# Kernel tuning notes

Measured on AMD Instinct MI355X. Metric: run time of the kernel, lower is better.

Reference implementation:

```python
import jax, jax.numpy as jnp
import numpy as np

H = 50  # hidden size hard-coded in the torch module


def _lstm_layer(x, W_ih, W_hh, b_ih, b_hh):
    """x: [B, T, D_in] -> outputs [B, T, H]. PyTorch gate order: i, f, g, o."""
    B = x.shape[0]
    # precompute input projection for all timesteps: [B, T, 4H]
    x_proj = jnp.einsum('btd,gd->btg', x, W_ih) + b_ih + b_hh
    x_proj = jnp.swapaxes(x_proj, 0, 1)  # time-major [T, B, 4H]

    def step(carry, xt):
        h, c = carry
        gates = xt + h @ W_hh.T  # [B, 4H]
        i, f, g, o = jnp.split(gates, 4, axis=-1)
        c = jax.nn.sigmoid(f) * c + jax.nn.sigmoid(i) * jnp.tanh(g)
        h = jax.nn.sigmoid(o) * jnp.tanh(c)
        return (h, c), h

    h0 = jnp.zeros((B, H), dtype=x.dtype)
    c0 = jnp.zeros((B, H), dtype=x.dtype)
    (_, _), hs = jax.lax.scan(step, (h0, c0), x_proj)
    return jnp.swapaxes(hs, 0, 1)  # [B, T, H]


def setup_inputs() -> dict:
    key = jax.random.key(0)
    ks = jax.random.split(key, 11)
    B, T = 4096, 512
    s = 1.0 / np.sqrt(H)  # torch LSTM init scale
    return {
        'x': jax.random.normal(ks[0], (B, T, 1), dtype=jnp.float32),
        'W_ih0': jax.random.normal(ks[1], (4 * H, 1), dtype=jnp.float32) * s,
        'W_hh0': jax.random.normal(ks[2], (4 * H, H), dtype=jnp.float32) * s,
        'b_ih0': jax.random.normal(ks[3], (4 * H,), dtype=jnp.float32) * s,
        'b_hh0': jax.random.normal(ks[4], (4 * H,), dtype=jnp.float32) * s,
        'W_ih1': jax.random.normal(ks[5], (4 * H, H), dtype=jnp.float32) * s,
        'W_hh1': jax.random.normal(ks[6], (4 * H, H), dtype=jnp.float32) * s,
        'b_ih1': jax.random.normal(ks[7], (4 * H,), dtype=jnp.float32) * s,
        'b_hh1': jax.random.normal(ks[8], (4 * H,), dtype=jnp.float32) * s,
        'W_fc': jax.random.normal(ks[9], (1, H), dtype=jnp.float32) * s,
        'b_fc': jax.random.normal(ks[10], (1,), dtype=jnp.float32) * s,
    }


def reference(x, W_ih0, W_hh0, b_ih0, b_hh0, W_ih1, W_hh1, b_ih1, b_hh1, W_fc, b_fc):
    h1 = _lstm_layer(x, W_ih0, W_hh0, b_ih0, b_hh0)   # [B, T, H]
    h2 = _lstm_layer(h1, W_ih1, W_hh1, b_ih1, b_hh1)  # [B, T, H]
    last = h2[:, -1, :]                                # [B, H]
    return last @ W_fc.T + b_fc                        # [B, 1]
```

## Files before the change

### kernel.cpp

```cpp
#include <hip/hip_runtime.h>


#define TT 512
#define HH 50
#define BT 16
#define NTHR 832
#define L2E 1.44269504f

typedef _Float16 half8 __attribute__((ext_vector_type(8)));
typedef float floatx4 __attribute__((ext_vector_type(4)));

static __device__ __forceinline__ float fexp2(float x) { return __builtin_amdgcn_exp2f(x); }
static __device__ __forceinline__ float frcp(float x)  { return __builtin_amdgcn_rcpf(x); }

static __device__ __forceinline__ float cell_update(float gi, float gf, float gg,
                                                    float go, float& c) {
    float Ei = fexp2(gi);
    float Eg = fexp2(gg);
    float Ef = fexp2(gf);
    float p1 = (1.0f + Ei) * (1.0f + Eg);
    float fe = 1.0f + Ef;
    float R  = frcp(fe * p1);
    c = R * (c * p1 + (1.0f - Eg) * fe);
    float cl = fminf(fmaxf(c, -18.0f), 18.0f);
    float Eo = fexp2(go);
    float Ec = fexp2(cl * (-2.0f * L2E));
    float Ro = frcp((1.0f + Eo) * (1.0f + Ec));
    return (1.0f - Ec) * Ro;
}

#define MFMA(a, b, c) __builtin_amdgcn_mfma_f32_16x16x32_f16((a), (b), (c), 0, 0, 0)

__global__ __launch_bounds__(NTHR, 4) void lstm_mfma(
    const float* __restrict__ x,
    const float* __restrict__ W_ih0, const float* __restrict__ W_hh0,
    const float* __restrict__ b_ih0, const float* __restrict__ b_hh0,
    const float* __restrict__ W_ih1, const float* __restrict__ W_hh1,
    const float* __restrict__ b_ih1, const float* __restrict__ b_hh1,
    const float* __restrict__ W_fc,  const float* __restrict__ b_fc,
    float* __restrict__ out)
{
    __shared__ __align__(16) _Float16 Hf[2][2048];
    __shared__ float xs[TT * BT];

    const int tid = threadIdx.x;
    const int ln  = tid & 63;
    const int wv  = tid >> 6;
    const int m   = ln & 15;
    const int q   = ln >> 4;
    const int b0g = blockIdx.x * BT;

    const float GSC[4] = { -L2E, -L2E, -2.0f * L2E, -L2E };

    for (int i = tid; i < BT * TT; i += NTHR) {
        int b = i & 15, t = i >> 4;
        xs[t * BT + b] = x[(size_t)(b0g + b) * TT + t];
    }
    for (int i = tid; i < 2 * 2048; i += NTHR) ((_Float16*)Hf)[i] = (_Float16)0.f;

    const int  uA   = 4 * wv + (m >> 2);
    const int  gA   = m & 3;
    const bool rokA = (uA < HH);
    const int  wrow = gA * HH + uA;
    const float sA  = GSC[gA];

    half8 a0[2];
    half8 a1[4];
#pragma unroll
    for (int ks = 0; ks < 2; ++ks) {
        half8 h8;
#pragma unroll
        for (int j = 0; j < 8; ++j) {
            int k = ks * 32 + q * 8 + j;
            float w = (rokA && k < HH) ? W_hh0[wrow * HH + k] : 0.f;
            h8[j] = (_Float16)(sA * w);
        }
        a0[ks] = h8;
    }
#pragma unroll
    for (int ks = 0; ks < 4; ++ks) {
        half8 h8;
#pragma unroll
        for (int j = 0; j < 8; ++j) {
            int k = ks * 32 + q * 8 + j;
            float w = 0.f;
            if (rokA) {
                if (k < HH)                      w = W_ih1[wrow * HH + k];
                else if (k >= 64 && k < 64 + HH) w = W_hh1[wrow * HH + (k - 64)];
            }
            h8[j] = (_Float16)(sA * w);
        }
        a1[ks] = h8;
    }

    const int  uC = 4 * wv + q;
    const bool vC = (uC < HH);
    float cc0[4], bw0[4], cc1[4];
#pragma unroll
    for (int g = 0; g < 4; ++g) {
        int rg = g * HH + (vC ? uC : 0);
        cc0[g] = vC ? GSC[g] * (b_ih0[rg] + b_hh0[rg]) : 0.f;
        bw0[g] = vC ? GSC[g] * W_ih0[rg] : 0.f;
        cc1[g] = vC ? GSC[g] * (b_ih1[rg] + b_hh1[rg]) : 0.f;
    }
    const int kh = uC & 63;
    const int widx = ((kh >> 5) * 64 + ((kh >> 3) & 3) * 16 + m) * 8 + (kh & 7);
    float c1 = 0.f, c2 = 0.f;

    __syncthreads();

#define ITER(ttv, P, DO_L0)                                               \
    {                                                                     \
        half8 b0 = *(const half8*)&Hf[(P)][(0 * 64 + ln) * 8];            \
        half8 b1 = *(const half8*)&Hf[(P)][(1 * 64 + ln) * 8];            \
        half8 b2 = *(const half8*)&Hf[(P)][(2 * 64 + ln) * 8];            \
        half8 b3 = *(const half8*)&Hf[(P)][(3 * 64 + ln) * 8];            \
        if (DO_L0) {                                                      \
            const float xv = xs[(ttv) * BT + m];                          \
            floatx4 acc;                                                  \
            _Pragma("unroll")                                             \
            for (int g = 0; g < 4; ++g) acc[g] = cc0[g] + bw0[g] * xv;    \
            acc = MFMA(a0[0], b0, acc);                                   \
            acc = MFMA(a0[1], b1, acc);                                   \
            float h = cell_update(acc[0], acc[1], acc[2], acc[3], c1);    \
            Hf[(P) ^ 1][widx] = (_Float16)h;                              \
        }                                                                 \
        {                                                                 \
            floatx4 acc;                                                  \
            _Pragma("unroll")                                             \
            for (int g = 0; g < 4; ++g) acc[g] = cc1[g];                  \
            acc = MFMA(a1[0], b0, acc);                                   \
            acc = MFMA(a1[1], b1, acc);                                   \
            acc = MFMA(a1[2], b2, acc);                                   \
            acc = MFMA(a1[3], b3, acc);                                   \
            float h = cell_update(acc[0], acc[1], acc[2], acc[3], c2);    \
            Hf[(P) ^ 1][widx + 1024] = (_Float16)h;                       \
        }                                                                 \
        __syncthreads();                                                  \
    }

    {
        const float xv = xs[m];
        float h = cell_update(cc0[0] + bw0[0] * xv, cc0[1] + bw0[1] * xv,
                              cc0[2] + bw0[2] * xv, cc0[3] + bw0[3] * xv, c1);
        Hf[1][widx] = (_Float16)h;
        __syncthreads();
    }

    for (int k = 1; k <= 255; ++k) {
        ITER(2 * k - 1, 1, true);
        ITER(2 * k,     0, true);
    }
    ITER(511, 1, true);
    ITER(512, 0, false);

    if (tid < BT) {
        float a = b_fc[0];
        for (int u = 0; u < HH; ++u) {
            int k = 64 + u;
            int idx = ((k >> 5) * 64 + ((k >> 3) & 3) * 16 + tid) * 8 + (k & 7);
            a = fmaf((float)Hf[1][idx], W_fc[u], a);
        }
        out[b0g + tid] = a;
    }
#undef ITER
}

extern "C" void kernel_launch(void* const* d_in, const int* in_sizes, int n_in,
                              void* d_out, int out_size, void* d_ws, size_t ws_size,
                              hipStream_t stream) {
    const float* x     = (const float*)d_in[0];
    const float* W_ih0 = (const float*)d_in[1];
    const float* W_hh0 = (const float*)d_in[2];
    const float* b_ih0 = (const float*)d_in[3];
    const float* b_hh0 = (const float*)d_in[4];
    const float* W_ih1 = (const float*)d_in[5];
    const float* W_hh1 = (const float*)d_in[6];
    const float* b_ih1 = (const float*)d_in[7];
    const float* b_hh1 = (const float*)d_in[8];
    const float* W_fc  = (const float*)d_in[9];
    const float* b_fc  = (const float*)d_in[10];
    float* out = (float*)d_out;

    dim3 grid(4096 / BT);
    dim3 block(NTHR);
    lstm_mfma<<<grid, block, 0, stream>>>(x, W_ih0, W_hh0, b_ih0, b_hh0,
                                          W_ih1, W_hh1, b_ih1, b_hh1,
                                          W_fc, b_fc, out);
}
```

Measured before the change: 409.0 us.

## Specialize waves per LSTM layer with multiple hidden-unit tiles per wave

```diff
diff --git a/kernel.cpp b/kernel.cpp
--- a/kernel.cpp
+++ b/kernel.cpp
@@ -4,7 +4,7 @@
 #define TT 512
 #define HH 50
 #define BT 16
-#define NTHR 832
+#define NTHR 512
 #define L2E 1.44269504f
 
 typedef _Float16 half8 __attribute__((ext_vector_type(8)));
@@ -31,7 +31,182 @@
 
 #define MFMA(a, b, c) __builtin_amdgcn_mfma_f32_16x16x32_f16((a), (b), (c), 0, 0, 0)
 
-__global__ __launch_bounds__(NTHR, 4) void lstm_mfma(
+template<int NJ>
+static __device__ __forceinline__ void run_l0(
+    int tbase, int ln, _Float16 (*Hf)[2048], const float* xs,
+    const float* __restrict__ W_ih0, const float* __restrict__ W_hh0,
+    const float* __restrict__ b_ih0, const float* __restrict__ b_hh0)
+{
+    const int m = ln & 15, q = ln >> 4;
+    const float GSC[4] = { -L2E, -L2E, -2.0f * L2E, -L2E };
+
+    half8 a0[NJ][2];
+    float cc0[NJ][4], bw0[NJ][4], c[NJ];
+    int   widx[NJ];
+#pragma unroll
+    for (int j = 0; j < NJ; ++j) {
+        const int  tau  = tbase + j;
+        const int  uA   = 4 * tau + (m >> 2);
+        const int  gA   = m & 3;
+        const bool rokA = (uA < HH);
+        const int  wrow = gA * HH + uA;
+        const float sA  = GSC[gA];
+#pragma unroll
+        for (int ks = 0; ks < 2; ++ks) {
+            half8 h8;
+#pragma unroll
+            for (int jj = 0; jj < 8; ++jj) {
+                int k = ks * 32 + q * 8 + jj;
+                float w = (rokA && k < HH) ? W_hh0[wrow * HH + k] : 0.f;
+                h8[jj] = (_Float16)(sA * w);
+            }
+            a0[j][ks] = h8;
+        }
+        const int  uC = 4 * tau + q;
+        const bool vC = (uC < HH);
+#pragma unroll
+        for (int g = 0; g < 4; ++g) {
+            int rg = g * HH + (vC ? uC : 0);
+            cc0[j][g] = vC ? GSC[g] * (b_ih0[rg] + b_hh0[rg]) : 0.f;
+            bw0[j][g] = vC ? GSC[g] * W_ih0[rg] : 0.f;
+        }
+        const int kh = uC & 63;
+        widx[j] = ((kh >> 5) * 64 + ((kh >> 3) & 3) * 16 + m) * 8 + (kh & 7);
+        c[j] = 0.f;
+    }
+
+    __syncthreads();
+
+    {
+        const float xv = xs[m];
+#pragma unroll
+        for (int j = 0; j < NJ; ++j) {
+            float h = cell_update(cc0[j][0] + bw0[j][0] * xv, cc0[j][1] + bw0[j][1] * xv,
+                                  cc0[j][2] + bw0[j][2] * xv, cc0[j][3] + bw0[j][3] * xv,
+                                  c[j]);
+            Hf[1][widx[j]] = (_Float16)h;
+        }
+        __syncthreads();
+    }
+
+#define ITER0(ttv, P)                                                       \
+    {                                                                       \
+        half8 b0 = *(const half8*)&Hf[(P)][(0 * 64 + ln) * 8];              \
+        half8 b1 = *(const half8*)&Hf[(P)][(1 * 64 + ln) * 8];              \
+        const float xv = xs[(ttv) * BT + m];                                \
+        floatx4 acc[NJ];                                                    \
+        _Pragma("unroll")                                                   \
+        for (int j = 0; j < NJ; ++j) {                                      \
+            floatx4 a;                                                      \
+            _Pragma("unroll")                                               \
+            for (int g = 0; g < 4; ++g) a[g] = cc0[j][g] + bw0[j][g] * xv;  \
+            a = MFMA(a0[j][0], b0, a);                                      \
+            a = MFMA(a0[j][1], b1, a);                                      \
+            acc[j] = a;                                                     \
+        }                                                                   \
+        _Pragma("unroll")                                                   \
+        for (int j = 0; j < NJ; ++j) {                                      \
+            float h = cell_update(acc[j][0], acc[j][1], acc[j][2], acc[j][3], c[j]); \
+            Hf[(P) ^ 1][widx[j]] = (_Float16)h;                             \
+        }                                                                   \
+        __syncthreads();                                                    \
+    }
+
+    for (int k = 1; k <= 255; ++k) {
+        ITER0(2 * k - 1, 1);
+        ITER0(2 * k, 0);
+    }
+    ITER0(511, 1);
+    __syncthreads();
+#undef ITER0
+}
+
+template<int NJ>
+static __device__ __forceinline__ void run_l1(
+    int tbase, int ln, _Float16 (*Hf)[2048],
+    const float* __restrict__ W_ih1, const float* __restrict__ W_hh1,
+    const float* __restrict__ b_ih1, const float* __restrict__ b_hh1)
+{
+    const int m = ln & 15, q = ln >> 4;
+    const float GSC[4] = { -L2E, -L2E, -2.0f * L2E, -L2E };
+
+    half8 a1[NJ][4];
+    float cc1[NJ][4], c[NJ];
+    int   widx[NJ];
+#pragma unroll
+    for (int j = 0; j < NJ; ++j) {
+        const int  tau  = tbase + j;
+        const int  uA   = 4 * tau + (m >> 2);
+        const int  gA   = m & 3;
+        const bool rokA = (uA < HH);
+        const int  wrow = gA * HH + uA;
+        const float sA  = GSC[gA];
+#pragma unroll
+        for (int ks = 0; ks < 4; ++ks) {
+            half8 h8;
+#pragma unroll
+            for (int jj = 0; jj < 8; ++jj) {
+                int k = ks * 32 + q * 8 + jj;
+                float w = 0.f;
+                if (rokA) {
+                    if (k < HH)                      w = W_ih1[wrow * HH + k];
+                    else if (k >= 64 && k < 64 + HH) w = W_hh1[wrow * HH + (k - 64)];
+                }
+                h8[jj] = (_Float16)(sA * w);
+            }
+            a1[j][ks] = h8;
+        }
+        const int  uC = 4 * tau + q;
+        const bool vC = (uC < HH);
+#pragma unroll
+        for (int g = 0; g < 4; ++g) {
+            int rg = g * HH + (vC ? uC : 0);
+            cc1[j][g] = vC ? GSC[g] * (b_ih1[rg] + b_hh1[rg]) : 0.f;
+        }
+        const int kh = uC & 63;
+        widx[j] = ((kh >> 5) * 64 + ((kh >> 3) & 3) * 16 + m) * 8 + (kh & 7) + 1024;
+        c[j] = 0.f;
+    }
+
+    __syncthreads();
+    __syncthreads();
+
+#define ITER1(P)                                                            \
+    {                                                                       \
+        half8 b0 = *(const half8*)&Hf[(P)][(0 * 64 + ln) * 8];              \
+        half8 b1 = *(const half8*)&Hf[(P)][(1 * 64 + ln) * 8];              \
+        half8 b2 = *(const half8*)&Hf[(P)][(2 * 64 + ln) * 8];              \
+        half8 b3 = *(const half8*)&Hf[(P)][(3 * 64 + ln) * 8];              \
+        floatx4 acc[NJ];                                                    \
+        _Pragma("unroll")                                                   \
+        for (int j = 0; j < NJ; ++j) {                                      \
+            floatx4 a;                                                      \
+            _Pragma("unroll")                                               \
+            for (int g = 0; g < 4; ++g) a[g] = cc1[j][g];                   \
+            a = MFMA(a1[j][0], b0, a);                                      \
+            a = MFMA(a1[j][1], b1, a);                                      \
+            a = MFMA(a1[j][2], b2, a);                                      \
+            a = MFMA(a1[j][3], b3, a);                                      \
+            acc[j] = a;                                                     \
+        }                                                                   \
+        _Pragma("unroll")                                                   \
+        for (int j = 0; j < NJ; ++j) {                                      \
+            float h = cell_update(acc[j][0], acc[j][1], acc[j][2], acc[j][3], c[j]); \
+            Hf[(P) ^ 1][widx[j]] = (_Float16)h;                             \
+        }                                                                   \
+        __syncthreads();                                                    \
+    }
+
+    for (int k = 1; k <= 255; ++k) {
+        ITER1(1);
+        ITER1(0);
+    }
+    ITER1(1);
+    ITER1(0);
+#undef ITER1
+}
+
+__global__ __launch_bounds__(NTHR, 2) void lstm_mfma(
     const float* __restrict__ x,
     const float* __restrict__ W_ih0, const float* __restrict__ W_hh0,
     const float* __restrict__ b_ih0, const float* __restrict__ b_hh0,
@@ -46,11 +221,7 @@
     const int tid = threadIdx.x;
     const int ln  = tid & 63;
     const int wv  = tid >> 6;
-    const int m   = ln & 15;
-    const int q   = ln >> 4;
     const int b0g = blockIdx.x * BT;
-
-    const float GSC[4] = { -L2E, -L2E, -2.0f * L2E, -L2E };
 
     for (int i = tid; i < BT * TT; i += NTHR) {
         int b = i & 15, t = i >> 4;
@@ -58,101 +229,14 @@
     }
     for (int i = tid; i < 2 * 2048; i += NTHR) ((_Float16*)Hf)[i] = (_Float16)0.f;
 
-    const int  uA   = 4 * wv + (m >> 2);
-    const int  gA   = m & 3;
-    const bool rokA = (uA < HH);
-    const int  wrow = gA * HH + uA;
-    const float sA  = GSC[gA];
-
-    half8 a0[2];
-    half8 a1[4];
-#pragma unroll
-    for (int ks = 0; ks < 2; ++ks) {
-        half8 h8;
-#pragma unroll
-        for (int j = 0; j < 8; ++j) {
-            int k = ks * 32 + q * 8 + j;
-            float w = (rokA && k < HH) ? W_hh0[wrow * HH + k] : 0.f;
-            h8[j] = (_Float16)(sA * w);
-        }
-        a0[ks] = h8;
-    }
-#pragma unroll
-    for (int ks = 0; ks < 4; ++ks) {
-        half8 h8;
-#pragma unroll
-        for (int j = 0; j < 8; ++j) {
-            int k = ks * 32 + q * 8 + j;
-            float w = 0.f;
-            if (rokA) {
-                if (k < HH)                      w = W_ih1[wrow * HH + k];
-                else if (k >= 64 && k < 64 + HH) w = W_hh1[wrow * HH + (k - 64)];
-            }
-            h8[j] = (_Float16)(sA * w);
-        }
-        a1[ks] = h8;
-    }
-
-    const int  uC = 4 * wv + q;
-    const bool vC = (uC < HH);
-    float cc0[4], bw0[4], cc1[4];
-#pragma unroll
-    for (int g = 0; g < 4; ++g) {
-        int rg = g * HH + (vC ? uC : 0);
-        cc0[g] = vC ? GSC[g] * (b_ih0[rg] + b_hh0[rg]) : 0.f;
-        bw0[g] = vC ? GSC[g] * W_ih0[rg] : 0.f;
-        cc1[g] = vC ? GSC[g] * (b_ih1[rg] + b_hh1[rg]) : 0.f;
-    }
-    const int kh = uC & 63;
-    const int widx = ((kh >> 5) * 64 + ((kh >> 3) & 3) * 16 + m) * 8 + (kh & 7);
-    float c1 = 0.f, c2 = 0.f;
-
-    __syncthreads();
-
-#define ITER(ttv, P, DO_L0)                                               \
-    {                                                                     \
-        half8 b0 = *(const half8*)&Hf[(P)][(0 * 64 + ln) * 8];            \
-        half8 b1 = *(const half8*)&Hf[(P)][(1 * 64 + ln) * 8];            \
-        half8 b2 = *(const half8*)&Hf[(P)][(2 * 64 + ln) * 8];            \
-        half8 b3 = *(const half8*)&Hf[(P)][(3 * 64 + ln) * 8];            \
-        if (DO_L0) {                                                      \
-            const float xv = xs[(ttv) * BT + m];                          \
-            floatx4 acc;                                                  \
-            _Pragma("unroll")                                             \
-            for (int g = 0; g < 4; ++g) acc[g] = cc0[g] + bw0[g] * xv;    \
-            acc = MFMA(a0[0], b0, acc);                                   \
-            acc = MFMA(a0[1], b1, acc);                                   \
-            float h = cell_update(acc[0], acc[1], acc[2], acc[3], c1);    \
-            Hf[(P) ^ 1][widx] = (_Float16)h;                              \
-        }                                                                 \
-        {                                                                 \
-            floatx4 acc;                                                  \
-            _Pragma("unroll")                                             \
-            for (int g = 0; g < 4; ++g) acc[g] = cc1[g];                  \
-            acc = MFMA(a1[0], b0, acc);                                   \
-            acc = MFMA(a1[1], b1, acc);                                   \
-            acc = MFMA(a1[2], b2, acc);                                   \
-            acc = MFMA(a1[3], b3, acc);                                   \
-            float h = cell_update(acc[0], acc[1], acc[2], acc[3], c2);    \
-            Hf[(P) ^ 1][widx + 1024] = (_Float16)h;                       \
-        }                                                                 \
-        __syncthreads();                                                  \
-    }
-
-    {
-        const float xv = xs[m];
-        float h = cell_update(cc0[0] + bw0[0] * xv, cc0[1] + bw0[1] * xv,
-                              cc0[2] + bw0[2] * xv, cc0[3] + bw0[3] * xv, c1);
-        Hf[1][widx] = (_Float16)h;
-        __syncthreads();
-    }
-
-    for (int k = 1; k <= 255; ++k) {
-        ITER(2 * k - 1, 1, true);
-        ITER(2 * k,     0, true);
-    }
-    ITER(511, 1, true);
-    ITER(512, 0, false);
+    if (wv == 0)
+        run_l0<4>(0, ln, Hf, xs, W_ih0, W_hh0, b_ih0, b_hh0);
+    else if (wv < 4)
+        run_l0<3>(wv == 1 ? 4 : (wv == 2 ? 7 : 10), ln, Hf, xs, W_ih0, W_hh0, b_ih0, b_hh0);
+    else if (wv == 5)
+        run_l1<4>(3, ln, Hf, W_ih1, W_hh1, b_ih1, b_hh1);
+    else
+        run_l1<3>(wv == 4 ? 0 : (wv == 6 ? 7 : 10), ln, Hf, W_ih1, W_hh1, b_ih1, b_hh1);
 
     if (tid < BT) {
         float a = b_fc[0];
@@ -163,7 +247,6 @@
         }
         out[b0g + tid] = a;
     }
-#undef ITER
 }
 
 extern "C" void kernel_launch(void* const* d_in, const int* in_sizes, int n_in,
```

New measurement: 376.1 us. -8.1%, faster.
